# Optimization experiments

Hardware: AMD Instinct MI355X
Metric: run time of the kernel (lower is better)

## Reference

```python
import jax, jax.numpy as jnp
import numpy as np

D_MODEL, D_STATE, D_CONV, EXPAND = 1024, 16, 4, 2
D_INNER = EXPAND * D_MODEL
B, L = 1, 2048
LN_EPS = 1e-5


def setup_inputs() -> dict:
    key = jax.random.key(0)
    ks = jax.random.split(key, 10)
    s = lambda fan_in: 1.0 / np.sqrt(fan_in)
    return {
        "x": jax.random.normal(ks[0], (B, L, D_MODEL), dtype=jnp.float32),
        "in_proj_w": jax.random.uniform(ks[1], (2 * D_INNER, D_MODEL), jnp.float32, -s(D_MODEL), s(D_MODEL)),
        "conv_w": jax.random.uniform(ks[2], (D_INNER, 1, D_CONV), jnp.float32, -s(D_CONV), s(D_CONV)),
        "conv_b": jax.random.uniform(ks[3], (D_INNER,), jnp.float32, -s(D_CONV), s(D_CONV)),
        "x_proj_w": jax.random.uniform(ks[4], (2 * D_STATE + 1, D_INNER), jnp.float32, -s(D_INNER), s(D_INNER)),
        "dt_w": jax.random.uniform(ks[5], (D_INNER,), jnp.float32, -1.0, 1.0),
        "dt_b": jax.random.uniform(ks[6], (D_INNER,), jnp.float32, -1.0, 1.0),
        "A_log": jnp.log(jnp.broadcast_to(jnp.arange(1, D_STATE + 1, dtype=jnp.float32), (D_INNER, D_STATE))),
        "D": jnp.ones((D_INNER,), jnp.float32),
        "out_proj_w": jax.random.uniform(ks[7], (D_MODEL, D_INNER), jnp.float32, -s(D_INNER), s(D_INNER)),
        "ln_g": jnp.ones((D_MODEL,), jnp.float32),
        "ln_b": jnp.zeros((D_MODEL,), jnp.float32),
    }


def _layernorm(x, g, b):
    mu = jnp.mean(x, axis=-1, keepdims=True)
    var = jnp.var(x, axis=-1, keepdims=True)
    return (x - mu) * jax.lax.rsqrt(var + LN_EPS) * g + b


def _selective_scan(xc, delta, A, Bm, Cm, Dp):
    # xc,delta: (B,L,D); A: (D,N); Bm,Cm: (B,L,N); Dp: (D,)
    deltaA = jnp.exp(delta[..., None] * A)                 # (B,L,D,N)
    deltaBx = delta[..., None] * Bm[:, :, None, :] * xc[..., None]  # (B,L,D,N)
    h0 = jnp.zeros((xc.shape[0], xc.shape[2], A.shape[1]), xc.dtype)

    def step(h, inp):
        dA_t, dBx_t, c_t = inp                             # (B,D,N),(B,D,N),(B,N)
        h = dA_t * h + dBx_t
        y_t = jnp.einsum('bdn,bn->bd', h, c_t)
        return h, y_t

    xs = (jnp.swapaxes(deltaA, 0, 1), jnp.swapaxes(deltaBx, 0, 1), jnp.swapaxes(Cm, 0, 1))
    _, ys = jax.lax.scan(step, h0, xs)                     # ys: (L,B,D)
    y = jnp.swapaxes(ys, 0, 1)
    return y + xc * Dp


def reference(x, in_proj_w, conv_w, conv_b, x_proj_w, dt_w, dt_b, A_log, D, out_proj_w, ln_g, ln_b):
    residual = x
    xn = _layernorm(x, ln_g, ln_b)
    xz = jnp.einsum('bld,ed->ble', xn, in_proj_w)          # (B,L,2*D_INNER)
    x_proj, z = jnp.split(xz, 2, axis=-1)
    # depthwise causal conv1d (torch pads d_conv-1 both sides then truncates to L == left-pad only)
    lhs = jnp.swapaxes(x_proj, 1, 2)                       # (B,D,L)
    xc = jax.lax.conv_general_dilated(
        lhs, conv_w, window_strides=(1,), padding=[(D_CONV - 1, 0)],
        dimension_numbers=('NCH', 'OIH', 'NCH'), feature_group_count=D_INNER)
    xc = jnp.swapaxes(xc + conv_b[None, :, None], 1, 2)    # (B,L,D)
    xc = jax.nn.silu(xc)
    x_ssm = jnp.einsum('bld,ed->ble', xc, x_proj_w)        # (B,L,2N+1)
    dt, Bm, Cm = jnp.split(x_ssm, [1, 1 + D_STATE], axis=-1)
    delta = jax.nn.softplus(dt * dt_w + dt_b)              # (B,L,1)*(D,) -> (B,L,D)
    A = -jnp.exp(A_log.astype(jnp.float32))
    y = _selective_scan(xc, delta, A, Bm, Cm, D)
    y = y * jax.nn.silu(z)
    out = jnp.einsum('bld,ed->ble', y, out_proj_w)
    return out + residual
```

## Files before the change

### kernel.cpp

```cpp
#include <hip/hip_runtime.h>
#include <hip/hip_bf16.h>

#define L_SEQ 2048
#define DM    1024
#define DI    2048
#define NST   16
#define NC    64
#define LC    (L_SEQ/NC)
#define KSPLIT 16
#define KCH   (DI/KSPLIT)
#define KS_OUT 4

typedef __bf16 bf16x8 __attribute__((ext_vector_type(8)));
typedef float  f32x4  __attribute__((ext_vector_type(4)));
typedef unsigned short u16x4 __attribute__((ext_vector_type(4)));

__device__ inline unsigned short f2bf(float f){
  __hip_bfloat16 h = __float2bfloat16(f);
  return *reinterpret_cast<unsigned short*>(&h);
}
__device__ inline float bf2f(unsigned short u){
  unsigned int x = ((unsigned int)u)<<16;
  float f; __builtin_memcpy(&f,&x,4); return f;
}

__device__ inline void gload16(const void* g, void* l){
  __builtin_amdgcn_global_load_lds(
      (const __attribute__((address_space(1))) void*)g,
      (__attribute__((address_space(3))) void*)l, 16, 0, 0);
}

__device__ inline float silu(float v){ return v/(1.f + __expf(-v)); }

__global__ __launch_bounds__(256) void ln_cvt(
    const float* __restrict__ x, const float* __restrict__ g,
    const float* __restrict__ b, __hip_bfloat16* __restrict__ xn,
    const float* __restrict__ w1, const float* __restrict__ w2,
    __hip_bfloat16* __restrict__ o1, __hip_bfloat16* __restrict__ o2)
{
  int tid = threadIdx.x;
  if (blockIdx.x < L_SEQ){
    int t = blockIdx.x;
    const float4 v = ((const float4*)(x + (size_t)t*DM))[tid];
    float s  = v.x+v.y+v.z+v.w;
    float ss = v.x*v.x+v.y*v.y+v.z*v.z+v.w*v.w;
    #pragma unroll
    for (int m=1;m<64;m<<=1){ s += __shfl_xor(s,m); ss += __shfl_xor(ss,m); }
    __shared__ float sb[4], ssb[4];
    if ((tid&63)==0){ sb[tid>>6]=s; ssb[tid>>6]=ss; }
    __syncthreads();
    s  = sb[0]+sb[1]+sb[2]+sb[3];
    ss = ssb[0]+ssb[1]+ssb[2]+ssb[3];
    float mu  = s*(1.f/DM);
    float var = ss*(1.f/DM) - mu*mu;
    float rs  = rsqrtf(var + 1e-5f);
    float4 gg = ((const float4*)g)[tid], bb = ((const float4*)b)[tid];
    u16x4 o = { f2bf((v.x-mu)*rs*gg.x+bb.x), f2bf((v.y-mu)*rs*gg.y+bb.y),
                f2bf((v.z-mu)*rs*gg.z+bb.z), f2bf((v.w-mu)*rs*gg.w+bb.w) };
    *(u16x4*)((unsigned short*)xn + (size_t)t*DM + tid*4) = o;
  } else {
    int i = ((blockIdx.x - L_SEQ)*256 + tid)*4;
    const int n1 = 2*DI*DM;
    const float* src; unsigned short* dst; int j;
    if (i < n1){ src = w1; dst = (unsigned short*)o1; j = i; }
    else       { src = w2; dst = (unsigned short*)o2; j = i - n1; }
    float4 v = *(const float4*)(src + j);
    u16x4 o = { f2bf(v.x), f2bf(v.y), f2bf(v.z), f2bf(v.w) };
    *(u16x4*)(dst + j) = o;
  }
}

template<int EPI>
__global__ __launch_bounds__(256) void gemm_bt(
    const __hip_bfloat16* __restrict__ A, const __hip_bfloat16* __restrict__ B,
    void* __restrict__ Cout, int M, int N, int K)
{
  __shared__ __align__(16) unsigned short As[2][128*64];
  __shared__ __align__(16) unsigned short Bs[2][128*64];
  int tid = threadIdx.x;
  int w = tid>>6, l = tid&63;
  int nwg = gridDim.x*gridDim.y;
  int bid = blockIdx.y*gridDim.x + blockIdx.x;
  int cpx = nwg>>3;
  int nb  = (bid&7)*cpx + (bid>>3);
  int m0 = (nb/gridDim.x)*128, n0 = (nb%gridDim.x)*128;
  int wr = (w>>1)*64, wc = (w&1)*64;
  int lr = l&15, lk = l>>4;
  int kchunk = K/gridDim.z;
  int kbase = blockIdx.z*kchunk;
  int ktiles = kchunk/64;
  f32x4 acc[4][4] = {};

  int cbase = w*64 + l;
  auto stage = [&](int buf, int k0){
    #pragma unroll
    for (int i=0;i<4;i++){
      int cc = i*256 + cbase;
      int row = cc>>3, q = cc&7;
      gload16(A + (size_t)(m0+row)*K + k0 + q*8, (char*)&As[buf][0] + (size_t)(i*256 + w*64)*16);
      gload16(B + (size_t)(n0+row)*K + k0 + q*8, (char*)&Bs[buf][0] + (size_t)(i*256 + w*64)*16);
    }
  };

  stage(0, kbase);
  __syncthreads();
  int cur = 0;
  for (int kt=0; kt<ktiles; ++kt){
    if (kt+1 < ktiles) stage(cur^1, kbase + (kt+1)*64);
    #pragma unroll
    for (int kk=0;kk<2;kk++){
      bf16x8 af[4], bfb[4];
      #pragma unroll
      for (int i=0;i<4;i++){
        af[i]  = *(const bf16x8*)&As[cur][(wr + i*16 + lr)*64 + kk*32 + lk*8];
        bfb[i] = *(const bf16x8*)&Bs[cur][(wc + i*16 + lr)*64 + kk*32 + lk*8];
      }
      #pragma unroll
      for (int i=0;i<4;i++)
        #pragma unroll
        for (int j=0;j<4;j++)
          acc[i][j] = __builtin_amdgcn_mfma_f32_16x16x32_bf16(af[i], bfb[j], acc[i][j], 0,0,0);
    }
    if (kt+1 < ktiles){ __syncthreads(); cur ^= 1; }
  }

  #pragma unroll
  for (int i=0;i<4;i++){
    #pragma unroll
    for (int j=0;j<4;j++){
      #pragma unroll
      for (int r=0;r<4;r++){
        int row = m0 + wr + i*16 + lk*4 + r;
        int col = n0 + wc + j*16 + lr;
        size_t off = (size_t)row*N + col;
        float v = acc[i][j][r];
        if (EPI==2) ((__hip_bfloat16*)Cout)[off] = __float2bfloat16(v);
        else        ((float*)Cout + (size_t)blockIdx.z*M*N)[off] = v;
      }
    }
  }
}

__global__ __launch_bounds__(256) void reduce_res(
    const float* __restrict__ part, const float* __restrict__ R,
    float* __restrict__ out, int n)
{
  size_t i = (size_t)(blockIdx.x*256 + threadIdx.x)*4;
  if (i >= (size_t)n) return;
  float4 a = *(const float4*)(part + i);
  float4 b = *(const float4*)(part + (size_t)n + i);
  float4 c = *(const float4*)(part + 2*(size_t)n + i);
  float4 d = *(const float4*)(part + 3*(size_t)n + i);
  float4 r = *(const float4*)(R + i);
  float4 o = { a.x+b.x+c.x+d.x+r.x, a.y+b.y+c.y+d.y+r.y,
               a.z+b.z+c.z+d.z+r.z, a.w+b.w+c.w+d.w+r.w };
  *(float4*)(out + i) = o;
}

__global__ __launch_bounds__(256) void gemm2_kernel(
    const unsigned short* __restrict__ xzb, const float* __restrict__ cw,
    const float* __restrict__ cb, const float* __restrict__ xpw,
    float* __restrict__ part)
{
  __shared__ float Xs[16*68];
  __shared__ float Ws[33*68];
  int tid = threadIdx.x;
  int t0 = blockIdx.x*16;
  int kbase = blockIdx.y*KCH;
  int tt = tid&15, g = tid>>4;
  float a0=0.f, a1=0.f, a2=0.f;
  for (int k0=kbase; k0<kbase+KCH; k0+=64){
    __syncthreads();
    {
      int ct = tid>>4, kq = tid&15;
      int t = t0+ct, k = k0+kq*4;
      float4 c0 = *(const float4*)&cw[(k+0)*4];
      float4 c1 = *(const float4*)&cw[(k+1)*4];
      float4 c2 = *(const float4*)&cw[(k+2)*4];
      float4 bb = *(const float4*)&cb[k];
      float4 c3 = *(const float4*)&cw[(k+3)*4];
      float s0=bb.x, s1=bb.y, s2=bb.z, s3=bb.w;
      #pragma unroll
      for (int j=0;j<4;j++){
        int tj = t-3+j;
        if (tj >= 0){
          u16x4 xv = *(const u16x4*)&xzb[(size_t)tj*2*DI + k];
          float w0 = (j==0)?c0.x:(j==1)?c0.y:(j==2)?c0.z:c0.w;
          float w1 = (j==0)?c1.x:(j==1)?c1.y:(j==2)?c1.z:c1.w;
          float w2 = (j==0)?c2.x:(j==1)?c2.y:(j==2)?c2.z:c2.w;
          float w3 = (j==0)?c3.x:(j==1)?c3.y:(j==2)?c3.z:c3.w;
          s0 = fmaf(bf2f(xv[0]), w0, s0); s1 = fmaf(bf2f(xv[1]), w1, s1);
          s2 = fmaf(bf2f(xv[2]), w2, s2); s3 = fmaf(bf2f(xv[3]), w3, s3);
        }
      }
      float4 v = { silu(s0), silu(s1), silu(s2), silu(s3) };
      *(float4*)&Xs[ct*68 + kq*4] = v;
    }
    for (int i=tid; i<528; i+=256){
      int e = i>>4, kq = i&15;
      float4 v = *(const float4*)&xpw[(size_t)e*DI + k0 + kq*4];
      *(float4*)&Ws[e*68 + kq*4] = v;
    }
    __syncthreads();
    #pragma unroll 4
    for (int kq=0;kq<16;kq++){
      float4 xv = *(const float4*)&Xs[tt*68 + kq*4];
      float4 w0 = *(const float4*)&Ws[g*68 + kq*4];
      float4 w1 = *(const float4*)&Ws[(g+16)*68 + kq*4];
      a0 += xv.x*w0.x + xv.y*w0.y + xv.z*w0.z + xv.w*w0.w;
      a1 += xv.x*w1.x + xv.y*w1.y + xv.z*w1.z + xv.w*w1.w;
      if (g==0){
        float4 w2 = *(const float4*)&Ws[32*68 + kq*4];
        a2 += xv.x*w2.x + xv.y*w2.y + xv.z*w2.z + xv.w*w2.w;
      }
    }
  }
  size_t base = (size_t)blockIdx.y*L_SEQ*33 + (size_t)(t0+tt)*33;
  part[base + g]      = a0;
  part[base + g + 16] = a1;
  if (g==0) part[base + 32] = a2;
}

__global__ __launch_bounds__(256) void gemm2_reduce(
    const float* __restrict__ part, float* __restrict__ xssm)
{
  int i = blockIdx.x*256 + threadIdx.x;
  if (i >= L_SEQ*33) return;
  float s = 0.f;
  #pragma unroll
  for (int c=0;c<KSPLIT;c++) s += part[(size_t)c*L_SEQ*33 + i];
  xssm[i] = s;
}

__global__ __launch_bounds__(256) void scan1(
    const float* __restrict__ xssm, const unsigned short* __restrict__ xzb,
    const float* __restrict__ cw, const float* __restrict__ cb,
    const float* __restrict__ dtw, const float* __restrict__ dtb,
    const float* __restrict__ Alog, const float* __restrict__ Dp,
    unsigned short* __restrict__ ylocal, float* __restrict__ hpart,
    float* __restrict__ cend)
{
  int d = blockIdx.x*256 + threadIdx.x;
  int c = blockIdx.y;
  float A[16];
  #pragma unroll
  for (int q=0;q<4;q++){
    float4 al = *(const float4*)&Alog[d*16 + q*4];
    A[q*4+0] = -__expf(al.x); A[q*4+1] = -__expf(al.y);
    A[q*4+2] = -__expf(al.z); A[q*4+3] = -__expf(al.w);
  }
  float4 cwv = *(const float4*)&cw[d*4];
  float cbv = cb[d];
  float wd = dtw[d], bd = dtb[d], Dd = Dp[d];
  float h[16];
  #pragma unroll
  for (int n=0;n<16;n++) h[n] = 0.f;
  float cum = 0.f;
  int t0 = c*LC;
  float xw0=0.f, xw1=0.f, xw2=0.f;
  if (t0 > 0){
    xw0 = bf2f(xzb[(size_t)(t0-3)*2*DI + d]);
    xw1 = bf2f(xzb[(size_t)(t0-2)*2*DI + d]);
    xw2 = bf2f(xzb[(size_t)(t0-1)*2*DI + d]);
  }
  for (int t=t0; t<t0+LC; ++t){
    const float* row = xssm + (size_t)t*33;
    float xin = bf2f(xzb[(size_t)t*2*DI + d]);
    float cv = fmaf(xin, cwv.w, fmaf(xw2, cwv.z, fmaf(xw1, cwv.y, fmaf(xw0, cwv.x, cbv))));
    xw0=xw1; xw1=xw2; xw2=xin;
    float xv = silu(cv);
    float u = fmaf(row[0], wd, bd);
    float delta = (u > 20.f) ? u : __logf(1.f + __expf(u));
    cum += delta;
    float dx = delta * xv;
    float y  = Dd * xv;
    #pragma unroll
    for (int n=0;n<16;n++){
      float dA = __expf(delta * A[n]);
      h[n] = fmaf(dA, h[n], row[1+n]*dx);
      y = fmaf(h[n], row[17+n], y);
    }
    ylocal[(size_t)t*DI + d] = f2bf(y);
  }
  #pragma unroll
  for (int n=0;n<16;n++)
    hpart[((size_t)c*16 + n)*DI + d] = h[n];
  cend[(size_t)c*DI + d] = cum;
}

__global__ __launch_bounds__(64) void scanfix(
    const float* __restrict__ hpart, const float* __restrict__ cend,
    const float* __restrict__ Alog, float* __restrict__ hinit)
{
  int gid = blockIdx.x*64 + threadIdx.x;
  int d = gid & (DI-1), n = gid >> 11;
  float A = -__expf(Alog[d*16 + n]);
  float h = 0.f;
  for (int cb=0; cb<NC; cb+=8){
    float cv[8], hp[8];
    #pragma unroll
    for (int j=0;j<8;j++){
      cv[j] = cend[(size_t)(cb+j)*DI + d];
      hp[j] = hpart[((size_t)(cb+j)*16 + n)*DI + d];
    }
    #pragma unroll
    for (int j=0;j<8;j++){
      hinit[((size_t)(cb+j)*16 + n)*DI + d] = h;
      h = fmaf(__expf(A*cv[j]), h, hp[j]);
    }
  }
}

__global__ __launch_bounds__(256) void scan2g(
    const float* __restrict__ xssm, const unsigned short* __restrict__ xzb,
    const float* __restrict__ cw, const float* __restrict__ cb,
    const float* __restrict__ dtw, const float* __restrict__ dtb,
    const float* __restrict__ Alog, const float* __restrict__ hinit,
    const unsigned short* __restrict__ ylocal, __hip_bfloat16* __restrict__ gb)
{
  int d = blockIdx.x*256 + threadIdx.x;
  int c = blockIdx.y;
  float A[16], h0[16];
  #pragma unroll
  for (int q=0;q<4;q++){
    float4 al = *(const float4*)&Alog[d*16 + q*4];
    A[q*4+0] = -__expf(al.x); A[q*4+1] = -__expf(al.y);
    A[q*4+2] = -__expf(al.z); A[q*4+3] = -__expf(al.w);
  }
  #pragma unroll
  for (int n=0;n<16;n++) h0[n] = hinit[((size_t)c*16 + n)*DI + d];
  float4 cwv = *(const float4*)&cw[d*4];
  float cbv = cb[d];
  float wd = dtw[d], bd = dtb[d];
  float cum = 0.f;
  int t0 = c*LC;
  float xw0=0.f, xw1=0.f, xw2=0.f;
  if (t0 > 0){
    xw0 = bf2f(xzb[(size_t)(t0-3)*2*DI + d]);
    xw1 = bf2f(xzb[(size_t)(t0-2)*2*DI + d]);
    xw2 = bf2f(xzb[(size_t)(t0-1)*2*DI + d]);
  }
  for (int t=t0; t<t0+LC; ++t){
    const float* row = xssm + (size_t)t*33;
    float xin = bf2f(xzb[(size_t)t*2*DI + d]);
    float cv = fmaf(xin, cwv.w, fmaf(xw2, cwv.z, fmaf(xw1, cwv.y, fmaf(xw0, cwv.x, cbv))));
    xw0=xw1; xw1=xw2; xw2=xin;
    float u = fmaf(row[0], wd, bd);
    float delta = (u > 20.f) ? u : __logf(1.f + __expf(u));
    cum += delta;
    float corr = 0.f;
    #pragma unroll
    for (int n=0;n<16;n++)
      corr = fmaf(__expf(A[n]*cum)*h0[n], row[17+n], corr);
    float y = bf2f(ylocal[(size_t)t*DI + d]) + corr;
    float z = bf2f(xzb[(size_t)t*2*DI + DI + d]);
    gb[(size_t)t*DI + d] = __float2bfloat16(y*silu(z));
  }
}

extern "C" void kernel_launch(void* const* d_in, const int* in_sizes, int n_in,
                              void* d_out, int out_size, void* d_ws, size_t ws_size,
                              hipStream_t stream)
{
  const float* x    = (const float*)d_in[0];
  const float* w_in = (const float*)d_in[1];
  const float* cw   = (const float*)d_in[2];
  const float* cb   = (const float*)d_in[3];
  const float* xpw  = (const float*)d_in[4];
  const float* dtw  = (const float*)d_in[5];
  const float* dtb  = (const float*)d_in[6];
  const float* Alog = (const float*)d_in[7];
  const float* Dp   = (const float*)d_in[8];
  const float* w_out= (const float*)d_in[9];
  const float* lng  = (const float*)d_in[10];
  const float* lnb  = (const float*)d_in[11];
  float* out = (float*)d_out;

  char* p = (char*)d_ws;
  auto carve = [&](size_t bytes)->char*{ char* r = p; p += (bytes + 255) & ~(size_t)255; return r; };
  __hip_bfloat16* xn  = (__hip_bfloat16*)carve((size_t)L_SEQ*DM*2);
  __hip_bfloat16* w1b = (__hip_bfloat16*)carve((size_t)2*DI*DM*2);
  __hip_bfloat16* w3b = (__hip_bfloat16*)carve((size_t)DM*DI*2);
  unsigned short* xzb = (unsigned short*)carve((size_t)L_SEQ*2*DI*2);
  unsigned short* ylocal=(unsigned short*)carve((size_t)L_SEQ*DI*2);
  float* xssm = (float*)carve((size_t)L_SEQ*33*4);
  float* hpart= (float*)carve((size_t)NC*NST*DI*4);
  float* hinit= (float*)carve((size_t)NC*NST*DI*4);
  float* cend = (float*)carve((size_t)NC*DI*4);
  float* opart= (float*)carve((size_t)KS_OUT*L_SEQ*DM*4);
  __hip_bfloat16* gb = (__hip_bfloat16*)w1b;
  float* part = hpart;

  ln_cvt<<<L_SEQ + (2*DI*DM + DM*DI)/1024, 256, 0, stream>>>(x, lng, lnb, xn, w_in, w_out, w1b, w3b);
  gemm_bt<2><<<dim3((2*DI)/128, L_SEQ/128, 1), 256, 0, stream>>>(xn, w1b, xzb, L_SEQ, 2*DI, DM);
  gemm2_kernel<<<dim3(L_SEQ/16, KSPLIT), 256, 0, stream>>>(xzb, cw, cb, xpw, part);
  gemm2_reduce<<<(L_SEQ*33 + 255)/256, 256, 0, stream>>>(part, xssm);
  scan1<<<dim3(DI/256, NC), 256, 0, stream>>>(xssm, xzb, cw, cb, dtw, dtb, Alog, Dp, ylocal, hpart, cend);
  scanfix<<<(DI*NST)/64, 64, 0, stream>>>(hpart, cend, Alog, hinit);
  scan2g<<<dim3(DI/256, NC), 256, 0, stream>>>(xssm, xzb, cw, cb, dtw, dtb, Alog, hinit, ylocal, gb);
  gemm_bt<0><<<dim3(DM/128, L_SEQ/128, KS_OUT), 256, 0, stream>>>(gb, w3b, opart, L_SEQ, DM, DI);
  reduce_res<<<(L_SEQ*DM)/1024, 256, 0, stream>>>(opart, x, out, L_SEQ*DM);
}
```

Baseline: 158.3 us.

## Fuse weight bf16 conversion into GEMM staging and recompute scan in second pass

Drops the separate fp32-to-bf16 weight conversion kernel; both GEMMs now load fp32 weights into registers and convert while writing to LDS. The chunked scan is restructured so the first pass only produces chunk-end states, and the second pass reruns the recurrence from corrected initial states, which removes the ylocal intermediate buffer. This trades extra fp32 weight reads per GEMM tile and register staging for fewer kernels and less intermediate memory traffic.

```diff
diff --git a/kernel.cpp b/kernel.cpp
--- a/kernel.cpp
+++ b/kernel.cpp
@@ -32,47 +32,33 @@
 
 __device__ inline float silu(float v){ return v/(1.f + __expf(-v)); }
 
-__global__ __launch_bounds__(256) void ln_cvt(
+__global__ __launch_bounds__(256) void ln_kernel(
     const float* __restrict__ x, const float* __restrict__ g,
-    const float* __restrict__ b, __hip_bfloat16* __restrict__ xn,
-    const float* __restrict__ w1, const float* __restrict__ w2,
-    __hip_bfloat16* __restrict__ o1, __hip_bfloat16* __restrict__ o2)
-{
-  int tid = threadIdx.x;
-  if (blockIdx.x < L_SEQ){
-    int t = blockIdx.x;
-    const float4 v = ((const float4*)(x + (size_t)t*DM))[tid];
-    float s  = v.x+v.y+v.z+v.w;
-    float ss = v.x*v.x+v.y*v.y+v.z*v.z+v.w*v.w;
-    #pragma unroll
-    for (int m=1;m<64;m<<=1){ s += __shfl_xor(s,m); ss += __shfl_xor(ss,m); }
-    __shared__ float sb[4], ssb[4];
-    if ((tid&63)==0){ sb[tid>>6]=s; ssb[tid>>6]=ss; }
-    __syncthreads();
-    s  = sb[0]+sb[1]+sb[2]+sb[3];
-    ss = ssb[0]+ssb[1]+ssb[2]+ssb[3];
-    float mu  = s*(1.f/DM);
-    float var = ss*(1.f/DM) - mu*mu;
-    float rs  = rsqrtf(var + 1e-5f);
-    float4 gg = ((const float4*)g)[tid], bb = ((const float4*)b)[tid];
-    u16x4 o = { f2bf((v.x-mu)*rs*gg.x+bb.x), f2bf((v.y-mu)*rs*gg.y+bb.y),
-                f2bf((v.z-mu)*rs*gg.z+bb.z), f2bf((v.w-mu)*rs*gg.w+bb.w) };
-    *(u16x4*)((unsigned short*)xn + (size_t)t*DM + tid*4) = o;
-  } else {
-    int i = ((blockIdx.x - L_SEQ)*256 + tid)*4;
-    const int n1 = 2*DI*DM;
-    const float* src; unsigned short* dst; int j;
-    if (i < n1){ src = w1; dst = (unsigned short*)o1; j = i; }
-    else       { src = w2; dst = (unsigned short*)o2; j = i - n1; }
-    float4 v = *(const float4*)(src + j);
-    u16x4 o = { f2bf(v.x), f2bf(v.y), f2bf(v.z), f2bf(v.w) };
-    *(u16x4*)(dst + j) = o;
-  }
+    const float* __restrict__ b, __hip_bfloat16* __restrict__ xn)
+{
+  int t = blockIdx.x, tid = threadIdx.x;
+  const float4 v = ((const float4*)(x + (size_t)t*DM))[tid];
+  float s  = v.x+v.y+v.z+v.w;
+  float ss = v.x*v.x+v.y*v.y+v.z*v.z+v.w*v.w;
+  #pragma unroll
+  for (int m=1;m<64;m<<=1){ s += __shfl_xor(s,m); ss += __shfl_xor(ss,m); }
+  __shared__ float sb[4], ssb[4];
+  if ((tid&63)==0){ sb[tid>>6]=s; ssb[tid>>6]=ss; }
+  __syncthreads();
+  s  = sb[0]+sb[1]+sb[2]+sb[3];
+  ss = ssb[0]+ssb[1]+ssb[2]+ssb[3];
+  float mu  = s*(1.f/DM);
+  float var = ss*(1.f/DM) - mu*mu;
+  float rs  = rsqrtf(var + 1e-5f);
+  float4 gg = ((const float4*)g)[tid], bb = ((const float4*)b)[tid];
+  u16x4 o = { f2bf((v.x-mu)*rs*gg.x+bb.x), f2bf((v.y-mu)*rs*gg.y+bb.y),
+              f2bf((v.z-mu)*rs*gg.z+bb.z), f2bf((v.w-mu)*rs*gg.w+bb.w) };
+  *(u16x4*)((unsigned short*)xn + (size_t)t*DM + tid*4) = o;
 }
 
 template<int EPI>
 __global__ __launch_bounds__(256) void gemm_bt(
-    const __hip_bfloat16* __restrict__ A, const __hip_bfloat16* __restrict__ B,
+    const __hip_bfloat16* __restrict__ A, const float* __restrict__ Bw,
     void* __restrict__ Cout, int M, int N, int K)
 {
   __shared__ __align__(16) unsigned short As[2][128*64];
@@ -91,22 +77,41 @@
   int ktiles = kchunk/64;
   f32x4 acc[4][4] = {};
 
-  int cbase = w*64 + l;
-  auto stage = [&](int buf, int k0){
+  float4 breg[8];
+  auto stageA = [&](int buf, int k0){
     #pragma unroll
     for (int i=0;i<4;i++){
-      int cc = i*256 + cbase;
+      int cc = i*256 + w*64 + l;
       int row = cc>>3, q = cc&7;
-      gload16(A + (size_t)(m0+row)*K + k0 + q*8, (char*)&As[buf][0] + (size_t)(i*256 + w*64)*16);
-      gload16(B + (size_t)(n0+row)*K + k0 + q*8, (char*)&Bs[buf][0] + (size_t)(i*256 + w*64)*16);
+      gload16(A + (size_t)(m0+row)*K + k0 + q*8,
+              (char*)&As[buf][0] + (size_t)(i*256 + w*64)*16);
     }
   };
-
-  stage(0, kbase);
+  auto issueB = [&](int k0){
+    #pragma unroll
+    for (int i=0;i<8;i++){
+      int qid = i*256 + tid;
+      int row = qid>>4, q = qid&15;
+      breg[i] = *(const float4*)&Bw[(size_t)(n0+row)*K + k0 + q*4];
+    }
+  };
+  auto writeB = [&](int buf){
+    #pragma unroll
+    for (int i=0;i<8;i++){
+      int qid = i*256 + tid;
+      int row = qid>>4, q = qid&15;
+      u16x4 o = { f2bf(breg[i].x), f2bf(breg[i].y), f2bf(breg[i].z), f2bf(breg[i].w) };
+      *(u16x4*)&Bs[buf][row*64 + q*4] = o;
+    }
+  };
+
+  issueB(kbase);
+  stageA(0, kbase);
+  writeB(0);
   __syncthreads();
   int cur = 0;
   for (int kt=0; kt<ktiles; ++kt){
-    if (kt+1 < ktiles) stage(cur^1, kbase + (kt+1)*64);
+    if (kt+1 < ktiles){ issueB(kbase + (kt+1)*64); stageA(cur^1, kbase + (kt+1)*64); }
     #pragma unroll
     for (int kk=0;kk<2;kk++){
       bf16x8 af[4], bfb[4];
@@ -121,7 +126,7 @@
         for (int j=0;j<4;j++)
           acc[i][j] = __builtin_amdgcn_mfma_f32_16x16x32_bf16(af[i], bfb[j], acc[i][j], 0,0,0);
     }
-    if (kt+1 < ktiles){ __syncthreads(); cur ^= 1; }
+    if (kt+1 < ktiles){ writeB(cur^1); __syncthreads(); cur ^= 1; }
   }
 
   #pragma unroll
@@ -236,9 +241,8 @@
     const float* __restrict__ xssm, const unsigned short* __restrict__ xzb,
     const float* __restrict__ cw, const float* __restrict__ cb,
     const float* __restrict__ dtw, const float* __restrict__ dtb,
-    const float* __restrict__ Alog, const float* __restrict__ Dp,
-    unsigned short* __restrict__ ylocal, float* __restrict__ hpart,
-    float* __restrict__ cend)
+    const float* __restrict__ Alog,
+    float* __restrict__ hpart, float* __restrict__ cend)
 {
   int d = blockIdx.x*256 + threadIdx.x;
   int c = blockIdx.y;
@@ -251,7 +255,7 @@
   }
   float4 cwv = *(const float4*)&cw[d*4];
   float cbv = cb[d];
-  float wd = dtw[d], bd = dtb[d], Dd = Dp[d];
+  float wd = dtw[d], bd = dtb[d];
   float h[16];
   #pragma unroll
   for (int n=0;n<16;n++) h[n] = 0.f;
@@ -273,14 +277,11 @@
     float delta = (u > 20.f) ? u : __logf(1.f + __expf(u));
     cum += delta;
     float dx = delta * xv;
-    float y  = Dd * xv;
     #pragma unroll
     for (int n=0;n<16;n++){
       float dA = __expf(delta * A[n]);
       h[n] = fmaf(dA, h[n], row[1+n]*dx);
-      y = fmaf(h[n], row[17+n], y);
-    }
-    ylocal[(size_t)t*DI + d] = f2bf(y);
+    }
   }
   #pragma unroll
   for (int n=0;n<16;n++)
@@ -315,12 +316,12 @@
     const float* __restrict__ xssm, const unsigned short* __restrict__ xzb,
     const float* __restrict__ cw, const float* __restrict__ cb,
     const float* __restrict__ dtw, const float* __restrict__ dtb,
-    const float* __restrict__ Alog, const float* __restrict__ hinit,
-    const unsigned short* __restrict__ ylocal, __hip_bfloat16* __restrict__ gb)
+    const float* __restrict__ Alog, const float* __restrict__ Dp,
+    const float* __restrict__ hinit, __hip_bfloat16* __restrict__ gb)
 {
   int d = blockIdx.x*256 + threadIdx.x;
   int c = blockIdx.y;
-  float A[16], h0[16];
+  float A[16], h[16];
   #pragma unroll
   for (int q=0;q<4;q++){
     float4 al = *(const float4*)&Alog[d*16 + q*4];
@@ -328,11 +329,10 @@
     A[q*4+2] = -__expf(al.z); A[q*4+3] = -__expf(al.w);
   }
   #pragma unroll
-  for (int n=0;n<16;n++) h0[n] = hinit[((size_t)c*16 + n)*DI + d];
+  for (int n=0;n<16;n++) h[n] = hinit[((size_t)c*16 + n)*DI + d];
   float4 cwv = *(const float4*)&cw[d*4];
   float cbv = cb[d];
-  float wd = dtw[d], bd = dtb[d];
-  float cum = 0.f;
+  float wd = dtw[d], bd = dtb[d], Dd = Dp[d];
   int t0 = c*LC;
   float xw0=0.f, xw1=0.f, xw2=0.f;
   if (t0 > 0){
@@ -345,14 +345,17 @@
     float xin = bf2f(xzb[(size_t)t*2*DI + d]);
     float cv = fmaf(xin, cwv.w, fmaf(xw2, cwv.z, fmaf(xw1, cwv.y, fmaf(xw0, cwv.x, cbv))));
     xw0=xw1; xw1=xw2; xw2=xin;
+    float xv = silu(cv);
     float u = fmaf(row[0], wd, bd);
     float delta = (u > 20.f) ? u : __logf(1.f + __expf(u));
-    cum += delta;
-    float corr = 0.f;
-    #pragma unroll
-    for (int n=0;n<16;n++)
-      corr = fmaf(__expf(A[n]*cum)*h0[n], row[17+n], corr);
-    float y = bf2f(ylocal[(size_t)t*DI + d]) + corr;
+    float dx = delta * xv;
+    float y  = Dd * xv;
+    #pragma unroll
+    for (int n=0;n<16;n++){
+      float dA = __expf(delta * A[n]);
+      h[n] = fmaf(dA, h[n], row[1+n]*dx);
+      y = fmaf(h[n], row[17+n], y);
+    }
     float z = bf2f(xzb[(size_t)t*2*DI + DI + d]);
     gb[(size_t)t*DI + d] = __float2bfloat16(y*silu(z));
   }
@@ -379,25 +382,22 @@
   char* p = (char*)d_ws;
   auto carve = [&](size_t bytes)->char*{ char* r = p; p += (bytes + 255) & ~(size_t)255; return r; };
   __hip_bfloat16* xn  = (__hip_bfloat16*)carve((size_t)L_SEQ*DM*2);
-  __hip_bfloat16* w1b = (__hip_bfloat16*)carve((size_t)2*DI*DM*2);
-  __hip_bfloat16* w3b = (__hip_bfloat16*)carve((size_t)DM*DI*2);
   unsigned short* xzb = (unsigned short*)carve((size_t)L_SEQ*2*DI*2);
-  unsigned short* ylocal=(unsigned short*)carve((size_t)L_SEQ*DI*2);
+  __hip_bfloat16* gb  = (__hip_bfloat16*)carve((size_t)L_SEQ*DI*2);
   float* xssm = (float*)carve((size_t)L_SEQ*33*4);
   float* hpart= (float*)carve((size_t)NC*NST*DI*4);
   float* hinit= (float*)carve((size_t)NC*NST*DI*4);
   float* cend = (float*)carve((size_t)NC*DI*4);
   float* opart= (float*)carve((size_t)KS_OUT*L_SEQ*DM*4);
-  __hip_bfloat16* gb = (__hip_bfloat16*)w1b;
   float* part = hpart;
 
-  ln_cvt<<<L_SEQ + (2*DI*DM + DM*DI)/1024, 256, 0, stream>>>(x, lng, lnb, xn, w_in, w_out, w1b, w3b);
-  gemm_bt<2><<<dim3((2*DI)/128, L_SEQ/128, 1), 256, 0, stream>>>(xn, w1b, xzb, L_SEQ, 2*DI, DM);
+  ln_kernel<<<L_SEQ, 256, 0, stream>>>(x, lng, lnb, xn);
+  gemm_bt<2><<<dim3((2*DI)/128, L_SEQ/128, 1), 256, 0, stream>>>(xn, w_in, xzb, L_SEQ, 2*DI, DM);
   gemm2_kernel<<<dim3(L_SEQ/16, KSPLIT), 256, 0, stream>>>(xzb, cw, cb, xpw, part);
   gemm2_reduce<<<(L_SEQ*33 + 255)/256, 256, 0, stream>>>(part, xssm);
-  scan1<<<dim3(DI/256, NC), 256, 0, stream>>>(xssm, xzb, cw, cb, dtw, dtb, Alog, Dp, ylocal, hpart, cend);
+  scan1<<<dim3(DI/256, NC), 256, 0, stream>>>(xssm, xzb, cw, cb, dtw, dtb, Alog, hpart, cend);
   scanfix<<<(DI*NST)/64, 64, 0, stream>>>(hpart, cend, Alog, hinit);
-  scan2g<<<dim3(DI/256, NC), 256, 0, stream>>>(xssm, xzb, cw, cb, dtw, dtb, Alog, hinit, ylocal, gb);
-  gemm_bt<0><<<dim3(DM/128, L_SEQ/128, KS_OUT), 256, 0, stream>>>(gb, w3b, opart, L_SEQ, DM, DI);
+  scan2g<<<dim3(DI/256, NC), 256, 0, stream>>>(xssm, xzb, cw, cb, dtw, dtb, Alog, Dp, hinit, gb);
+  gemm_bt<0><<<dim3(DM/128, L_SEQ/128, KS_OUT), 256, 0, stream>>>(gb, w_out, opart, L_SEQ, DM, DI);
   reduce_res<<<(L_SEQ*DM)/1024, 256, 0, stream>>>(opart, x, out, L_SEQ*DM);
 }
```

Result: slower. 166.4 us (+5.1%).

## Replace split-K partial buffers and reduce kernels with atomic accumulation

Applied to the files above, without the earlier changes.

The two split-K reductions (x_proj and out_proj) now accumulate directly into the destination with float atomicAdd instead of writing partial buffers and running separate reduce kernels. The output is pre-seeded with the residual through a device-to-device memcpy, and xssm is zeroed with a memset. This removes two kernel launches and the round trip of partial sums through memory. In exchange it adds atomic traffic, including 4-way contention on each out_proj element, and floating-point summation order becomes nondeterministic. The out_proj GEMM is instantiated as EPI=1, and the EPI==2 check means that path takes the atomic branch.

```diff
diff --git a/kernel.cpp b/kernel.cpp
--- a/kernel.cpp
+++ b/kernel.cpp
@@ -135,32 +135,16 @@
         size_t off = (size_t)row*N + col;
         float v = acc[i][j][r];
         if (EPI==2) ((__hip_bfloat16*)Cout)[off] = __float2bfloat16(v);
-        else        ((float*)Cout + (size_t)blockIdx.z*M*N)[off] = v;
+        else        atomicAdd(&((float*)Cout)[off], v);
       }
     }
   }
-}
-
-__global__ __launch_bounds__(256) void reduce_res(
-    const float* __restrict__ part, const float* __restrict__ R,
-    float* __restrict__ out, int n)
-{
-  size_t i = (size_t)(blockIdx.x*256 + threadIdx.x)*4;
-  if (i >= (size_t)n) return;
-  float4 a = *(const float4*)(part + i);
-  float4 b = *(const float4*)(part + (size_t)n + i);
-  float4 c = *(const float4*)(part + 2*(size_t)n + i);
-  float4 d = *(const float4*)(part + 3*(size_t)n + i);
-  float4 r = *(const float4*)(R + i);
-  float4 o = { a.x+b.x+c.x+d.x+r.x, a.y+b.y+c.y+d.y+r.y,
-               a.z+b.z+c.z+d.z+r.z, a.w+b.w+c.w+d.w+r.w };
-  *(float4*)(out + i) = o;
 }
 
 __global__ __launch_bounds__(256) void gemm2_kernel(
     const unsigned short* __restrict__ xzb, const float* __restrict__ cw,
     const float* __restrict__ cb, const float* __restrict__ xpw,
-    float* __restrict__ part)
+    float* __restrict__ xssm)
 {
   __shared__ float Xs[16*68];
   __shared__ float Ws[33*68];
@@ -215,21 +199,10 @@
       }
     }
   }
-  size_t base = (size_t)blockIdx.y*L_SEQ*33 + (size_t)(t0+tt)*33;
-  part[base + g]      = a0;
-  part[base + g + 16] = a1;
-  if (g==0) part[base + 32] = a2;
-}
-
-__global__ __launch_bounds__(256) void gemm2_reduce(
-    const float* __restrict__ part, float* __restrict__ xssm)
-{
-  int i = blockIdx.x*256 + threadIdx.x;
-  if (i >= L_SEQ*33) return;
-  float s = 0.f;
-  #pragma unroll
-  for (int c=0;c<KSPLIT;c++) s += part[(size_t)c*L_SEQ*33 + i];
-  xssm[i] = s;
+  size_t base = (size_t)(t0+tt)*33;
+  atomicAdd(&xssm[base + g],      a0);
+  atomicAdd(&xssm[base + g + 16], a1);
+  if (g==0) atomicAdd(&xssm[base + 32], a2);
 }
 
 __global__ __launch_bounds__(256) void scan1(
@@ -387,17 +360,15 @@
   float* hpart= (float*)carve((size_t)NC*NST*DI*4);
   float* hinit= (float*)carve((size_t)NC*NST*DI*4);
   float* cend = (float*)carve((size_t)NC*DI*4);
-  float* opart= (float*)carve((size_t)KS_OUT*L_SEQ*DM*4);
   __hip_bfloat16* gb = (__hip_bfloat16*)w1b;
-  float* part = hpart;
-
+
+  hipMemcpyAsync(out, x, (size_t)L_SEQ*DM*4, hipMemcpyDeviceToDevice, stream);
+  hipMemsetAsync(xssm, 0, (size_t)L_SEQ*33*4, stream);
   ln_cvt<<<L_SEQ + (2*DI*DM + DM*DI)/1024, 256, 0, stream>>>(x, lng, lnb, xn, w_in, w_out, w1b, w3b);
   gemm_bt<2><<<dim3((2*DI)/128, L_SEQ/128, 1), 256, 0, stream>>>(xn, w1b, xzb, L_SEQ, 2*DI, DM);
-  gemm2_kernel<<<dim3(L_SEQ/16, KSPLIT), 256, 0, stream>>>(xzb, cw, cb, xpw, part);
-  gemm2_reduce<<<(L_SEQ*33 + 255)/256, 256, 0, stream>>>(part, xssm);
+  gemm2_kernel<<<dim3(L_SEQ/16, KSPLIT), 256, 0, stream>>>(xzb, cw, cb, xpw, xssm);
   scan1<<<dim3(DI/256, NC), 256, 0, stream>>>(xssm, xzb, cw, cb, dtw, dtb, Alog, Dp, ylocal, hpart, cend);
   scanfix<<<(DI*NST)/64, 64, 0, stream>>>(hpart, cend, Alog, hinit);
   scan2g<<<dim3(DI/256, NC), 256, 0, stream>>>(xssm, xzb, cw, cb, dtw, dtb, Alog, hinit, ylocal, gb);
-  gemm_bt<0><<<dim3(DM/128, L_SEQ/128, KS_OUT), 256, 0, stream>>>(gb, w3b, opart, L_SEQ, DM, DI);
-  reduce_res<<<(L_SEQ*DM)/1024, 256, 0, stream>>>(opart, x, out, L_SEQ*DM);
-}
+  gemm_bt<1><<<dim3(DM/128, L_SEQ/128, KS_OUT), 256, 0, stream>>>(gb, w3b, out, L_SEQ, DM, DI);
+}
```

Result: slower. 187.5 us (+18.4%).

## Drop split-K in out-projection GEMM and fuse residual add into epilogue

Applied to the files above, without the earlier changes.

Replaces the split-K out-projection GEMM plus separate reduce kernel with a single GEMM using 128x64 tiles that loops over the full K and adds the residual in its epilogue. This removes writing and re-reading four fp32 partial output buffers and one kernel launch. The trade-off is fewer blocks doing longer K loops, which lowers parallelism in the last GEMM.

```diff
diff --git a/kernel.cpp b/kernel.cpp
--- a/kernel.cpp
+++ b/kernel.cpp
@@ -9,7 +9,6 @@
 #define LC    (L_SEQ/NC)
 #define KSPLIT 16
 #define KCH   (DI/KSPLIT)
-#define KS_OUT 4
 
 typedef __bf16 bf16x8 __attribute__((ext_vector_type(8)));
 typedef float  f32x4  __attribute__((ext_vector_type(4)));
@@ -70,10 +69,9 @@
   }
 }
 
-template<int EPI>
 __global__ __launch_bounds__(256) void gemm_bt(
     const __hip_bfloat16* __restrict__ A, const __hip_bfloat16* __restrict__ B,
-    void* __restrict__ Cout, int M, int N, int K)
+    __hip_bfloat16* __restrict__ Cout, int M, int N, int K)
 {
   __shared__ __align__(16) unsigned short As[2][128*64];
   __shared__ __align__(16) unsigned short Bs[2][128*64];
@@ -86,9 +84,7 @@
   int m0 = (nb/gridDim.x)*128, n0 = (nb%gridDim.x)*128;
   int wr = (w>>1)*64, wc = (w&1)*64;
   int lr = l&15, lk = l>>4;
-  int kchunk = K/gridDim.z;
-  int kbase = blockIdx.z*kchunk;
-  int ktiles = kchunk/64;
+  int ktiles = K/64;
   f32x4 acc[4][4] = {};
 
   int cbase = w*64 + l;
@@ -102,11 +98,11 @@
     }
   };
 
-  stage(0, kbase);
+  stage(0, 0);
   __syncthreads();
   int cur = 0;
   for (int kt=0; kt<ktiles; ++kt){
-    if (kt+1 < ktiles) stage(cur^1, kbase + (kt+1)*64);
+    if (kt+1 < ktiles) stage(cur^1, (kt+1)*64);
     #pragma unroll
     for (int kk=0;kk<2;kk++){
       bf16x8 af[4], bfb[4];
@@ -132,29 +128,81 @@
       for (int r=0;r<4;r++){
         int row = m0 + wr + i*16 + lk*4 + r;
         int col = n0 + wc + j*16 + lr;
+        Cout[(size_t)row*N + col] = __float2bfloat16(acc[i][j][r]);
+      }
+    }
+  }
+}
+
+__global__ __launch_bounds__(256) void gemm_bt_res(
+    const __hip_bfloat16* __restrict__ A, const __hip_bfloat16* __restrict__ B,
+    const float* __restrict__ R, float* __restrict__ Cout, int M, int N, int K)
+{
+  __shared__ __align__(16) unsigned short As[2][128*64];
+  __shared__ __align__(16) unsigned short Bs[2][64*64];
+  int tid = threadIdx.x;
+  int w = tid>>6, l = tid&63;
+  int nwg = gridDim.x*gridDim.y;
+  int bid = blockIdx.y*gridDim.x + blockIdx.x;
+  int cpx = nwg>>3;
+  int nb  = (bid&7)*cpx + (bid>>3);
+  int m0 = (nb/gridDim.x)*128, n0 = (nb%gridDim.x)*64;
+  int wr = (w>>1)*64, wc = (w&1)*32;
+  int lr = l&15, lk = l>>4;
+  int ktiles = K/64;
+  f32x4 acc[4][2] = {};
+
+  auto stage = [&](int buf, int k0){
+    #pragma unroll
+    for (int i=0;i<4;i++){
+      int cc = i*256 + tid;
+      int row = cc>>3, q = cc&7;
+      gload16(A + (size_t)(m0+row)*K + k0 + q*8, (char*)&As[buf][0] + (size_t)cc*16);
+    }
+    #pragma unroll
+    for (int i=0;i<2;i++){
+      int cc = i*256 + tid;
+      int row = cc>>3, q = cc&7;
+      gload16(B + (size_t)(n0+row)*K + k0 + q*8, (char*)&Bs[buf][0] + (size_t)cc*16);
+    }
+  };
+
+  stage(0, 0);
+  __syncthreads();
+  int cur = 0;
+  for (int kt=0; kt<ktiles; ++kt){
+    if (kt+1 < ktiles) stage(cur^1, (kt+1)*64);
+    #pragma unroll
+    for (int kk=0;kk<2;kk++){
+      bf16x8 af[4], bfb[2];
+      #pragma unroll
+      for (int i=0;i<4;i++)
+        af[i]  = *(const bf16x8*)&As[cur][(wr + i*16 + lr)*64 + kk*32 + lk*8];
+      #pragma unroll
+      for (int j=0;j<2;j++)
+        bfb[j] = *(const bf16x8*)&Bs[cur][(wc + j*16 + lr)*64 + kk*32 + lk*8];
+      #pragma unroll
+      for (int i=0;i<4;i++)
+        #pragma unroll
+        for (int j=0;j<2;j++)
+          acc[i][j] = __builtin_amdgcn_mfma_f32_16x16x32_bf16(af[i], bfb[j], acc[i][j], 0,0,0);
+    }
+    if (kt+1 < ktiles){ __syncthreads(); cur ^= 1; }
+  }
+
+  #pragma unroll
+  for (int i=0;i<4;i++){
+    #pragma unroll
+    for (int j=0;j<2;j++){
+      #pragma unroll
+      for (int r=0;r<4;r++){
+        int row = m0 + wr + i*16 + lk*4 + r;
+        int col = n0 + wc + j*16 + lr;
         size_t off = (size_t)row*N + col;
-        float v = acc[i][j][r];
-        if (EPI==2) ((__hip_bfloat16*)Cout)[off] = __float2bfloat16(v);
-        else        ((float*)Cout + (size_t)blockIdx.z*M*N)[off] = v;
+        Cout[off] = acc[i][j][r] + R[off];
       }
     }
   }
-}
-
-__global__ __launch_bounds__(256) void reduce_res(
-    const float* __restrict__ part, const float* __restrict__ R,
-    float* __restrict__ out, int n)
-{
-  size_t i = (size_t)(blockIdx.x*256 + threadIdx.x)*4;
-  if (i >= (size_t)n) return;
-  float4 a = *(const float4*)(part + i);
-  float4 b = *(const float4*)(part + (size_t)n + i);
-  float4 c = *(const float4*)(part + 2*(size_t)n + i);
-  float4 d = *(const float4*)(part + 3*(size_t)n + i);
-  float4 r = *(const float4*)(R + i);
-  float4 o = { a.x+b.x+c.x+d.x+r.x, a.y+b.y+c.y+d.y+r.y,
-               a.z+b.z+c.z+d.z+r.z, a.w+b.w+c.w+d.w+r.w };
-  *(float4*)(out + i) = o;
 }
 
 __global__ __launch_bounds__(256) void gemm2_kernel(
@@ -387,17 +435,15 @@
   float* hpart= (float*)carve((size_t)NC*NST*DI*4);
   float* hinit= (float*)carve((size_t)NC*NST*DI*4);
   float* cend = (float*)carve((size_t)NC*DI*4);
-  float* opart= (float*)carve((size_t)KS_OUT*L_SEQ*DM*4);
   __hip_bfloat16* gb = (__hip_bfloat16*)w1b;
   float* part = hpart;
 
   ln_cvt<<<L_SEQ + (2*DI*DM + DM*DI)/1024, 256, 0, stream>>>(x, lng, lnb, xn, w_in, w_out, w1b, w3b);
-  gemm_bt<2><<<dim3((2*DI)/128, L_SEQ/128, 1), 256, 0, stream>>>(xn, w1b, xzb, L_SEQ, 2*DI, DM);
+  gemm_bt<<<dim3((2*DI)/128, L_SEQ/128), 256, 0, stream>>>(xn, w1b, (__hip_bfloat16*)xzb, L_SEQ, 2*DI, DM);
   gemm2_kernel<<<dim3(L_SEQ/16, KSPLIT), 256, 0, stream>>>(xzb, cw, cb, xpw, part);
   gemm2_reduce<<<(L_SEQ*33 + 255)/256, 256, 0, stream>>>(part, xssm);
   scan1<<<dim3(DI/256, NC), 256, 0, stream>>>(xssm, xzb, cw, cb, dtw, dtb, Alog, Dp, ylocal, hpart, cend);
   scanfix<<<(DI*NST)/64, 64, 0, stream>>>(hpart, cend, Alog, hinit);
   scan2g<<<dim3(DI/256, NC), 256, 0, stream>>>(xssm, xzb, cw, cb, dtw, dtb, Alog, hinit, ylocal, gb);
-  gemm_bt<0><<<dim3(DM/128, L_SEQ/128, KS_OUT), 256, 0, stream>>>(gb, w3b, opart, L_SEQ, DM, DI);
-  reduce_res<<<(L_SEQ*DM)/1024, 256, 0, stream>>>(opart, x, out, L_SEQ*DM);
-}
+  gemm_bt_res<<<dim3(DM/64, L_SEQ/128), 256, 0, stream>>>(gb, w3b, x, out, L_SEQ, DM, DI);
+}
```

New measurement: 166.1 us. 4.9% more time.
